# Kernel tuning notes

Hardware: AMD Instinct MI355X
Metric: run time of the kernel (lower is better)

## Reference

```python
import jax, jax.numpy as jnp
import numpy as np

N = 100_000   # nodes
E = 1_600_000 # edges
D = 32        # input_channels
H = 32        # hidden_inputs
C = 8         # output_channels
G = 64        # graphs in batch


def setup_inputs() -> dict:
    key = jax.random.key(0)
    ks = jax.random.split(key, 12)
    inp = {
        "x": jax.random.normal(ks[0], (N, D), dtype=jnp.float32),
        "edge_idx": jax.random.randint(ks[1], (2, E), 0, N, dtype=jnp.int64 if jax.config.jax_enable_x64 else jnp.int32),
        "edge_weight": jax.random.uniform(ks[2], (E,), dtype=jnp.float32),
        "batch": jnp.sort(jax.random.randint(ks[3], (N,), 0, G, dtype=jnp.int32)),
        # GCNConv weights (PyG: out = A_hat @ (x W) + b)
        "W1": jax.random.normal(ks[4], (D, H), dtype=jnp.float32) / np.sqrt(D),
        "b1": jnp.zeros((H,), dtype=jnp.float32),
        "W2": jax.random.normal(ks[5], (H, H), dtype=jnp.float32) / np.sqrt(H),
        "b2": jnp.zeros((H,), dtype=jnp.float32),
        "W3": jax.random.normal(ks[6], (H, H), dtype=jnp.float32) / np.sqrt(H),
        "b3": jnp.zeros((H,), dtype=jnp.float32),
        "Wout": jax.random.normal(ks[7], (H, C), dtype=jnp.float32) / np.sqrt(H),
        "bout": jnp.zeros((C,), dtype=jnp.float32),
    }
    return inp


def _gcn_norm(edge_idx, edge_weight, n_nodes):
    """Add self-loops (weight 1) and compute symmetric normalization,
    matching torch_geometric gcn_norm(add_self_loops=True)."""
    loop = jnp.arange(n_nodes, dtype=edge_idx.dtype)
    row = jnp.concatenate([edge_idx[0], loop])          # source j
    col = jnp.concatenate([edge_idx[1], loop])          # target i
    w = jnp.concatenate([edge_weight, jnp.ones((n_nodes,), edge_weight.dtype)])
    deg = jax.ops.segment_sum(w, col, num_segments=n_nodes)  # in-degree of targets
    dinv = jnp.where(deg > 0, jax.lax.rsqrt(deg), 0.0)
    norm = dinv[row] * w * dinv[col]
    return row, col, norm


def _gcn_conv(x, W, b, row, col, norm, n_nodes):
    h = x @ W                                   # [N, H] small GEMM
    msg = h[row] * norm[:, None]                # gather + scale  [E+N, H]
    agg = jax.ops.segment_sum(msg, col, num_segments=n_nodes)  # scatter-add
    return agg + b


def reference(x, edge_idx, edge_weight, batch, W1, b1, W2, b2, W3, b3, Wout, bout):
    n = x.shape[0]
    row, col, norm = _gcn_norm(edge_idx, edge_weight, n)
    h = jax.nn.relu(_gcn_conv(x, W1, b1, row, col, norm, n))
    h = jax.nn.relu(_gcn_conv(h, W2, b2, row, col, norm, n))
    h = jax.nn.relu(_gcn_conv(h, W3, b3, row, col, norm, n))
    # global mean pool over graphs
    sums = jax.ops.segment_sum(h, batch, num_segments=G)          # [G, H]
    cnts = jax.ops.segment_sum(jnp.ones((n,), h.dtype), batch, num_segments=G)
    pooled = sums / jnp.maximum(cnts, 1.0)[:, None]
    # dropout is identity in eval mode
    logits = pooled @ Wout + bout
    return jax.nn.log_softmax(logits, axis=1)
```

## Files before the change

### kernel.cpp

```cpp
#include <hip/hip_runtime.h>
#include <math.h>

#define NN 100000
#define NE 1600000
#define HD 32
#define NG 64
#define NC 8

#define P 256
#define PART 391
#define SCAP 7000
#define CH 8192
#define NBIN ((NE + CH - 1) / CH)
#define GEMM0_BLOCKS32 (NN / 32)
#define NORM_BLOCKS (NN * 8 / 256)

__device__ __forceinline__ float bf2f(unsigned short u) {
    return __uint_as_float(((unsigned int)u) << 16);
}
__device__ __forceinline__ unsigned short f2bf(float f) {
    unsigned int b = __float_as_uint(f);
    b = (b + 0x7FFFu + ((b >> 16) & 1u)) >> 16;
    return (unsigned short)b;
}

#if __has_builtin(__builtin_amdgcn_cvt_pk_f32_fp8) && __has_builtin(__builtin_amdgcn_cvt_pk_fp8_f32)
#define FP8_HW 1
#else
#define FP8_HW 0
#endif

__device__ __forceinline__ float e4m3f_sw(unsigned u) {
    unsigned code = u & 0x7fu;
    unsigned e = code >> 3;
    float v;
    if (e == 0) v = (float)code * 0.001953125f;
    else v = __uint_as_float(((e + 120u) << 23) | ((code & 7u) << 20));
    return (u & 0x80u) ? -v : v;
}
__device__ __forceinline__ unsigned f2e4m3_sw(float f) {
    unsigned s = (__float_as_uint(f) >> 31) << 7;
    float a = fminf(fabsf(f), 448.0f);
    unsigned code;
    if (a >= 0.015625f) {
        unsigned x = __float_as_uint(a);
        x += 0x0007FFFFu + ((x >> 20) & 1u);
        code = (((x >> 23) - 120u) << 3) | ((x >> 20) & 7u);
    } else {
        code = (unsigned)__float2int_rn(a * 512.0f);
    }
    return s | code;
}

__device__ __forceinline__ float4 fp8x4f(unsigned v) {
#if FP8_HW
    using floatx2 = __attribute__((ext_vector_type(2))) float;
    floatx2 lo = __builtin_amdgcn_cvt_pk_f32_fp8((int)v, false);
    floatx2 hi = __builtin_amdgcn_cvt_pk_f32_fp8((int)v, true);
    return make_float4(lo[0], lo[1], hi[0], hi[1]);
#else
    return make_float4(e4m3f_sw(v & 255), e4m3f_sw((v >> 8) & 255),
                       e4m3f_sw((v >> 16) & 255), e4m3f_sw(v >> 24));
#endif
}
__device__ __forceinline__ unsigned f4fp8(float a, float b, float c, float d) {
#if FP8_HW
    int pk = 0;
    pk = __builtin_amdgcn_cvt_pk_fp8_f32(a, b, pk, false);
    pk = __builtin_amdgcn_cvt_pk_fp8_f32(c, d, pk, true);
    return (unsigned)pk;
#else
    return f2e4m3_sw(a) | (f2e4m3_sw(b) << 8) | (f2e4m3_sw(c) << 16) | (f2e4m3_sw(d) << 24);
#endif
}

__global__ __launch_bounds__(1024) void k_bin_gemm0(const int* __restrict__ row,
                                                    const int* __restrict__ col,
                                                    const float* __restrict__ w,
                                                    int* __restrict__ pcnt,
                                                    uint2* __restrict__ staging,
                                                    const float* __restrict__ x,
                                                    const float* __restrict__ W1,
                                                    unsigned short* __restrict__ htmp) {
    int tid = threadIdx.x;
    if (blockIdx.x < NBIN) {
        __shared__ int hist[P];
        __shared__ int base_[P];
        int e0 = blockIdx.x * CH;
        int nrem = min(CH, NE - e0);
        if (tid < P) hist[tid] = 0;
        __syncthreads();
        for (int i = tid; i < nrem; i += 1024)
            atomicAdd(&hist[(unsigned)col[e0 + i] / PART], 1);
        __syncthreads();
        if (tid < P) {
            int h = hist[tid];
            base_[tid] = h ? atomicAdd(&pcnt[tid], h) : 0;
            hist[tid] = 0;
        }
        __syncthreads();
        for (int i = tid; i < nrem; i += 1024) {
            int c = col[e0 + i];
            int p = (unsigned)c / PART;
            int pos = base_[p] + atomicAdd(&hist[p], 1);
            uint2 v;
            v.x = (unsigned)(c - p * PART) | ((unsigned)row[e0 + i] << 9);
            v.y = __float_as_uint(w[e0 + i]);
            staging[(size_t)p * SCAP + pos] = v;
        }
    } else {
        __shared__ float sW[32 * 32];
        __shared__ float sX[32 * 32];
        int base = (blockIdx.x - NBIN) * 32;
        if (tid < 256) {
            ((float4*)sW)[tid] = ((const float4*)W1)[tid];
            ((float4*)sX)[tid] = ((const float4*)(x + (size_t)base * 32))[tid];
        }
        __syncthreads();
        int nl = tid >> 5, c = tid & 31;
        float acc = 0.0f;
#pragma unroll
        for (int k = 0; k < 32; ++k) acc = fmaf(sX[nl * 32 + k], sW[k * 32 + c], acc);
        htmp[(size_t)(base + nl) * 32 + c] = f2bf(acc);
    }
}

__global__ __launch_bounds__(512) void k_csr(const int* __restrict__ pcnt,
                                             const uint2* __restrict__ staging,
                                             int* __restrict__ off,
                                             int* __restrict__ cntg,
                                             float* __restrict__ dinv,
                                             const unsigned short* __restrict__ htmp,
                                             unsigned char* __restrict__ h1,
                                             unsigned* __restrict__ pairs) {
    __shared__ int spc[P];
    __shared__ int cnt_l[PART];
    __shared__ float wsum[PART];
    __shared__ int sc[PART];
    __shared__ float sdc[PART];
    __shared__ int cur[PART];
    int p = blockIdx.x, tid = threadIdx.x;
    if (tid < P) spc[tid] = pcnt[tid];
    __syncthreads();
#pragma unroll
    for (int d = 1; d < P; d <<= 1) {
        int t = 0;
        if (tid < P && tid >= d) t = spc[tid - d];
        __syncthreads();
        if (tid < P) spc[tid] += t;
        __syncthreads();
    }
    int m = pcnt[p];
    int pb = (p > 0) ? spc[p - 1] : 0;
    for (int i = tid; i < PART; i += 512) { cnt_l[i] = 0; wsum[i] = 0.0f; }
    __syncthreads();
    const uint2* st = staging + (size_t)p * SCAP;
    for (int i = tid; i < m; i += 512) {
        uint2 v = st[i];
        int cl = v.x & 511;
        atomicAdd(&cnt_l[cl], 1);
        atomicAdd(&wsum[cl], __uint_as_float(v.y));
    }
    __syncthreads();
    for (int i = tid; i < PART; i += 512) sc[i] = cnt_l[i];
    __syncthreads();
#pragma unroll
    for (int d = 1; d < 512; d <<= 1) {
        int t = 0;
        if (tid < PART && tid >= d) t = sc[tid - d];
        __syncthreads();
        if (tid < PART) sc[tid] += t;
        __syncthreads();
    }
    for (int i = tid; i < PART; i += 512) {
        int excl = sc[i] - cnt_l[i];
        cur[i] = excl;
        float dv = rsqrtf(1.0f + wsum[i]);
        sdc[i] = dv;
        int n = p * PART + i;
        if (n < NN) {
            off[n] = pb + excl;
            cntg[n] = cnt_l[i];
            dinv[n] = dv;
        }
    }
    __syncthreads();
    for (int u = tid; u < PART * 8; u += 512) {
        int i = u >> 3, q = u & 7;
        int n = p * PART + i;
        if (n < NN) {
            ushort4 hv = *((const ushort4*)(htmp + (size_t)n * 32) + q);
            float dv = sdc[i];
            *(unsigned*)(h1 + (size_t)n * 32 + q * 4) =
                f4fp8(dv * bf2f(hv.x), dv * bf2f(hv.y), dv * bf2f(hv.z), dv * bf2f(hv.w));
        }
    }
    unsigned* pr = pairs + pb;
    for (int ib = tid; ib < m; ib += 512 * 4) {
        uint2 v[4];
#pragma unroll
        for (int j = 0; j < 4; ++j) {
            int i = ib + j * 512;
            if (i < m) v[j] = st[i];
        }
#pragma unroll
        for (int j = 0; j < 4; ++j) {
            int i = ib + j * 512;
            if (i < m) {
                int cl = v[j].x & 511;
                int pos = atomicAdd(&cur[cl], 1);
                unsigned q = (unsigned)__float2int_rn(__uint_as_float(v[j].y) * 32768.0f);
                q = min(q, 32767u);
                pr[pos] = ((v[j].x >> 9) << 15) | q;
            }
        }
    }
}

#define NM_SCALE 3.0517578125e-5f
template <int MODE>
__global__ __launch_bounds__(256) void k_gather(const unsigned char* __restrict__ hb,
                                                const int* __restrict__ off,
                                                const int* __restrict__ cntg,
                                                const float* __restrict__ dinv,
                                                const unsigned* __restrict__ pairs,
                                                const float* __restrict__ bias,
                                                const float* __restrict__ Wn,
                                                unsigned char* __restrict__ hout,
                                                unsigned short* __restrict__ h3out) {
    __shared__ float sW[32 * 32];
    __shared__ float srow[32 * 33];
    int tid = threadIdx.x;
    if (MODE == 0) ((float4*)sW)[tid] = ((const float4*)Wn)[tid];
    int t = blockIdx.x * 256 + tid;
    int n = t >> 3, c4 = t & 7;
    int cn = cntg[n];
    const unsigned* pp = pairs + off[n];
    float di = dinv[n];
    unsigned hu = *(const unsigned*)(hb + (size_t)n * 32 + c4 * 4);
    float4 acc = fp8x4f(hu);
    int k = 0;
    for (; k + 8 <= cn; k += 8) {
        unsigned p[8];
#pragma unroll
        for (int j = 0; j < 8; ++j) p[j] = pp[k + j];
        unsigned v[8];
#pragma unroll
        for (int j = 0; j < 8; ++j)
            v[j] = *(const unsigned*)(hb + (size_t)(p[j] >> 15) * 32 + c4 * 4);
#pragma unroll
        for (int j = 0; j < 8; ++j) {
            float nm = (float)(p[j] & 32767u) * NM_SCALE;
            float4 f = fp8x4f(v[j]);
            acc.x = fmaf(nm, f.x, acc.x);
            acc.y = fmaf(nm, f.y, acc.y);
            acc.z = fmaf(nm, f.z, acc.z);
            acc.w = fmaf(nm, f.w, acc.w);
        }
    }
    for (; k + 4 <= cn; k += 4) {
        unsigned p[4];
#pragma unroll
        for (int j = 0; j < 4; ++j) p[j] = pp[k + j];
        unsigned v[4];
#pragma unroll
        for (int j = 0; j < 4; ++j)
            v[j] = *(const unsigned*)(hb + (size_t)(p[j] >> 15) * 32 + c4 * 4);
#pragma unroll
        for (int j = 0; j < 4; ++j) {
            float nm = (float)(p[j] & 32767u) * NM_SCALE;
            float4 f = fp8x4f(v[j]);
            acc.x = fmaf(nm, f.x, acc.x);
            acc.y = fmaf(nm, f.y, acc.y);
            acc.z = fmaf(nm, f.z, acc.z);
            acc.w = fmaf(nm, f.w, acc.w);
        }
    }
    for (; k < cn; ++k) {
        unsigned p = pp[k];
        unsigned v = *(const unsigned*)(hb + (size_t)(p >> 15) * 32 + c4 * 4);
        float nm = (float)(p & 32767u) * NM_SCALE;
        float4 f = fp8x4f(v);
        acc.x = fmaf(nm, f.x, acc.x);
        acc.y = fmaf(nm, f.y, acc.y);
        acc.z = fmaf(nm, f.z, acc.z);
        acc.w = fmaf(nm, f.w, acc.w);
    }
    int cb = c4 * 4;
    if (MODE == 0) {
        int ln = tid >> 3;
        srow[ln * 33 + cb + 0] = fmaxf(fmaf(di, acc.x, bias[cb + 0]), 0.0f);
        srow[ln * 33 + cb + 1] = fmaxf(fmaf(di, acc.y, bias[cb + 1]), 0.0f);
        srow[ln * 33 + cb + 2] = fmaxf(fmaf(di, acc.z, bias[cb + 2]), 0.0f);
        srow[ln * 33 + cb + 3] = fmaxf(fmaf(di, acc.w, bias[cb + 3]), 0.0f);
        __syncthreads();
        const float* rw = srow + ln * 33;
        float o0 = 0.f, o1 = 0.f, o2 = 0.f, o3 = 0.f;
#pragma unroll
        for (int kk = 0; kk < 32; ++kk) {
            float r = rw[kk];
            const float* wr = sW + kk * 32 + cb;
            o0 = fmaf(r, wr[0], o0);
            o1 = fmaf(r, wr[1], o1);
            o2 = fmaf(r, wr[2], o2);
            o3 = fmaf(r, wr[3], o3);
        }
        *(unsigned*)(hout + (size_t)n * 32 + cb) = f4fp8(di * o0, di * o1, di * o2, di * o3);
    } else {
        ushort4 ou;
        ou.x = f2bf(fmaxf(fmaf(di, acc.x, bias[cb + 0]), 0.0f));
        ou.y = f2bf(fmaxf(fmaf(di, acc.y, bias[cb + 1]), 0.0f));
        ou.z = f2bf(fmaxf(fmaf(di, acc.z, bias[cb + 2]), 0.0f));
        ou.w = f2bf(fmaxf(fmaf(di, acc.w, bias[cb + 3]), 0.0f));
        *((ushort4*)(h3out + (size_t)n * 32) + c4) = ou;
    }
}

__global__ __launch_bounds__(1024) void k_pool_head(const unsigned short* __restrict__ h3,
                                                    const int* __restrict__ batch,
                                                    const float* __restrict__ Wout,
                                                    const float* __restrict__ bout,
                                                    float* __restrict__ out) {
    int g = blockIdx.x;
    __shared__ int sb[2];
    if (threadIdx.x == 0) {
        int lo = 0, hi = NN;
        while (lo < hi) { int m = (lo + hi) >> 1; if (batch[m] < g) lo = m + 1; else hi = m; }
        sb[0] = lo;
        lo = 0; hi = NN;
        while (lo < hi) { int m = (lo + hi) >> 1; if (batch[m] < g + 1) lo = m + 1; else hi = m; }
        sb[1] = lo;
    }
    __syncthreads();
    int start = sb[0], end = sb[1];
    int c = threadIdx.x & 31, grp = threadIdx.x >> 5;
    float acc = 0.0f;
    for (int n = start + grp; n < end; n += 32)
        acc += bf2f(h3[(size_t)n * 32 + c]);
    __shared__ float red[32 * 32];
    red[grp * 32 + c] = acc;
    __syncthreads();
    __shared__ float pooled[32];
    if (threadIdx.x < 32) {
        float s = 0.0f;
#pragma unroll
        for (int gr = 0; gr < 32; ++gr) s += red[gr * 32 + threadIdx.x];
        pooled[threadIdx.x] = s / fmaxf((float)(end - start), 1.0f);
    }
    __syncthreads();
    __shared__ float slog[8];
    if (threadIdx.x < 8) {
        float l = bout[threadIdx.x];
#pragma unroll
        for (int k = 0; k < 32; ++k) l = fmaf(pooled[k], Wout[k * 8 + threadIdx.x], l);
        slog[threadIdx.x] = l;
    }
    __syncthreads();
    if (threadIdx.x < 8) {
        float m = slog[0];
#pragma unroll
        for (int i = 1; i < 8; ++i) m = fmaxf(m, slog[i]);
        float s = 0.0f;
#pragma unroll
        for (int i = 0; i < 8; ++i) s += expf(slog[i] - m);
        out[g * NC + threadIdx.x] = slog[threadIdx.x] - m - logf(s);
    }
}

extern "C" void kernel_launch(void* const* d_in, const int* in_sizes, int n_in,
                              void* d_out, int out_size, void* d_ws, size_t ws_size,
                              hipStream_t stream) {
    const float* x     = (const float*)d_in[0];
    const int*   eidx  = (const int*)d_in[1];
    const float* ew    = (const float*)d_in[2];
    const int*   batch = (const int*)d_in[3];
    const float* W1 = (const float*)d_in[4];
    const float* b1 = (const float*)d_in[5];
    const float* W2 = (const float*)d_in[6];
    const float* b2 = (const float*)d_in[7];
    const float* W3 = (const float*)d_in[8];
    const float* b3 = (const float*)d_in[9];
    const float* Wout = (const float*)d_in[10];
    const float* bout = (const float*)d_in[11];
    float* out = (float*)d_out;

    const int* row = eidx;
    const int* col = eidx + NE;

    unsigned char* h1 = (unsigned char*)d_ws;
    unsigned char* h2 = h1 + (size_t)NN * HD;
    unsigned short* h3 = (unsigned short*)(h2 + (size_t)NN * HD);
    unsigned* pairs = (unsigned*)(h3 + (size_t)NN * HD);
    uint2* staging = (uint2*)(pairs + NE);
    float* dinv = (float*)(staging + (size_t)P * SCAP);
    int* off  = (int*)(dinv + NN);
    int* cntg = off + NN;
    int* pcnt = cntg + NN;

    hipMemsetAsync(pcnt, 0, P * sizeof(int), stream);
    k_bin_gemm0<<<NBIN + GEMM0_BLOCKS32, 1024, 0, stream>>>(row, col, ew, pcnt, staging,
                                                            x, W1, h3 );
    k_csr<<<P, 512, 0, stream>>>(pcnt, staging, off, cntg, dinv, h3 , h1, pairs);
    k_gather<0><<<NORM_BLOCKS, 256, 0, stream>>>(h1, off, cntg, dinv, pairs, b1, W2,
                                                 h2, nullptr);
    k_gather<0><<<NORM_BLOCKS, 256, 0, stream>>>(h2, off, cntg, dinv, pairs, b2, W3,
                                                 h1, nullptr);
    k_gather<1><<<NORM_BLOCKS, 256, 0, stream>>>(h1, off, cntg, dinv, pairs, b3, nullptr,
                                                 nullptr, h3);
    k_pool_head<<<NG, 1024, 0, stream>>>(h3, batch, Wout, bout, out);
}
```

Baseline: 126.2 us.

## Stage gather pairs in LDS, cache bin columns, split pooling across blocks

Each gather block now loads its contiguous run of CSR pairs into shared memory in one coalesced pass, then reads neighbor indices from LDS, with a fallback to global when a block's edge count exceeds capacity. The binning kernel keeps the column indices in shared memory so they are not read from global a second time. Pooling is split into eight slices per graph that combine through atomics, followed by a separate single-block head kernel, which raises pooling parallelism at the cost of an extra launch and float atomics that make the summation order nondeterministic. The offset array gains a sentinel entry and the workspace layout shifts to make room for it.

```diff
diff --git a/kernel.cpp b/kernel.cpp
--- a/kernel.cpp
+++ b/kernel.cpp
@@ -14,6 +14,7 @@
 #define NBIN ((NE + CH - 1) / CH)
 #define GEMM0_BLOCKS32 (NN / 32)
 #define NORM_BLOCKS (NN * 8 / 256)
+#define CAPL 1024
 
 __device__ __forceinline__ float bf2f(unsigned short u) {
     return __uint_as_float(((unsigned int)u) << 16);
@@ -84,14 +85,18 @@
                                                     unsigned short* __restrict__ htmp) {
     int tid = threadIdx.x;
     if (blockIdx.x < NBIN) {
+        __shared__ int scol[CH];
         __shared__ int hist[P];
         __shared__ int base_[P];
         int e0 = blockIdx.x * CH;
         int nrem = min(CH, NE - e0);
         if (tid < P) hist[tid] = 0;
         __syncthreads();
-        for (int i = tid; i < nrem; i += 1024)
-            atomicAdd(&hist[(unsigned)col[e0 + i] / PART], 1);
+        for (int i = tid; i < nrem; i += 1024) {
+            int c = col[e0 + i];
+            scol[i] = c;
+            atomicAdd(&hist[(unsigned)c / PART], 1);
+        }
         __syncthreads();
         if (tid < P) {
             int h = hist[tid];
@@ -100,7 +105,7 @@
         }
         __syncthreads();
         for (int i = tid; i < nrem; i += 1024) {
-            int c = col[e0 + i];
+            int c = scol[i];
             int p = (unsigned)c / PART;
             int pos = base_[p] + atomicAdd(&hist[p], 1);
             uint2 v;
@@ -152,6 +157,7 @@
     }
     int m = pcnt[p];
     int pb = (p > 0) ? spc[p - 1] : 0;
+    if (p == P - 1 && tid == 0) off[NN] = pb + m;
     for (int i = tid; i < PART; i += 512) { cnt_l[i] = 0; wsum[i] = 0.0f; }
     __syncthreads();
     const uint2* st = staging + (size_t)p * SCAP;
@@ -218,6 +224,55 @@
 }
 
 #define NM_SCALE 3.0517578125e-5f
+
+#define GBODY(PAIR_AT)                                                              \
+    {                                                                               \
+        int k = 0;                                                                  \
+        for (; k + 8 <= cn; k += 8) {                                               \
+            unsigned pw[8];                                                         \
+            _Pragma("unroll") for (int j = 0; j < 8; ++j) pw[j] = PAIR_AT(k + j);   \
+            unsigned hv[8];                                                         \
+            _Pragma("unroll") for (int j = 0; j < 8; ++j)                           \
+                hv[j] = *(const unsigned*)(hb + (size_t)(pw[j] >> 15) * 32 + c4 * 4);\
+            _Pragma("unroll") for (int j = 0; j < 8; ++j) {                         \
+                float nm = (float)(pw[j] & 32767u) * NM_SCALE;                      \
+                float4 f = fp8x4f(hv[j]);                                           \
+                acc.x = fmaf(nm, f.x, acc.x);                                       \
+                acc.y = fmaf(nm, f.y, acc.y);                                       \
+                acc.z = fmaf(nm, f.z, acc.z);                                       \
+                acc.w = fmaf(nm, f.w, acc.w);                                       \
+            }                                                                       \
+        }                                                                           \
+        for (; k + 4 <= cn; k += 4) {                                               \
+            unsigned pw[4];                                                         \
+            _Pragma("unroll") for (int j = 0; j < 4; ++j) pw[j] = PAIR_AT(k + j);   \
+            unsigned hv[4];                                                         \
+            _Pragma("unroll") for (int j = 0; j < 4; ++j)                           \
+                hv[j] = *(const unsigned*)(hb + (size_t)(pw[j] >> 15) * 32 + c4 * 4);\
+            _Pragma("unroll") for (int j = 0; j < 4; ++j) {                         \
+                float nm = (float)(pw[j] & 32767u) * NM_SCALE;                      \
+                float4 f = fp8x4f(hv[j]);                                           \
+                acc.x = fmaf(nm, f.x, acc.x);                                       \
+                acc.y = fmaf(nm, f.y, acc.y);                                       \
+                acc.z = fmaf(nm, f.z, acc.z);                                       \
+                acc.w = fmaf(nm, f.w, acc.w);                                       \
+            }                                                                       \
+        }                                                                           \
+        for (; k < cn; ++k) {                                                       \
+            unsigned pw = PAIR_AT(k);                                               \
+            unsigned hv = *(const unsigned*)(hb + (size_t)(pw >> 15) * 32 + c4 * 4);\
+            float nm = (float)(pw & 32767u) * NM_SCALE;                             \
+            float4 f = fp8x4f(hv);                                                  \
+            acc.x = fmaf(nm, f.x, acc.x);                                           \
+            acc.y = fmaf(nm, f.y, acc.y);                                           \
+            acc.z = fmaf(nm, f.z, acc.z);                                           \
+            acc.w = fmaf(nm, f.w, acc.w);                                           \
+        }                                                                           \
+    }
+
+#define SPAIR_AT(i) spair[l0 + (i)]
+#define GPAIR_AT(i) pp[(i)]
+
 template <int MODE>
 __global__ __launch_bounds__(256) void k_gather(const unsigned char* __restrict__ hb,
                                                 const int* __restrict__ off,
@@ -230,61 +285,28 @@
                                                 unsigned short* __restrict__ h3out) {
     __shared__ float sW[32 * 32];
     __shared__ float srow[32 * 33];
+    __shared__ unsigned spair[CAPL];
     int tid = threadIdx.x;
     if (MODE == 0) ((float4*)sW)[tid] = ((const float4*)Wn)[tid];
+    int nb = blockIdx.x * 32;
+    int base = off[nb];
+    int mb = off[nb + 32] - base;
+    int mbc = min(mb, CAPL);
+    for (int i = tid; i < mbc; i += 256) spair[i] = pairs[base + i];
+    __syncthreads();
     int t = blockIdx.x * 256 + tid;
     int n = t >> 3, c4 = t & 7;
     int cn = cntg[n];
-    const unsigned* pp = pairs + off[n];
+    int offn = off[n];
+    int l0 = offn - base;
+    const unsigned* pp = pairs + offn;
     float di = dinv[n];
     unsigned hu = *(const unsigned*)(hb + (size_t)n * 32 + c4 * 4);
     float4 acc = fp8x4f(hu);
-    int k = 0;
-    for (; k + 8 <= cn; k += 8) {
-        unsigned p[8];
-#pragma unroll
-        for (int j = 0; j < 8; ++j) p[j] = pp[k + j];
-        unsigned v[8];
-#pragma unroll
-        for (int j = 0; j < 8; ++j)
-            v[j] = *(const unsigned*)(hb + (size_t)(p[j] >> 15) * 32 + c4 * 4);
-#pragma unroll
-        for (int j = 0; j < 8; ++j) {
-            float nm = (float)(p[j] & 32767u) * NM_SCALE;
-            float4 f = fp8x4f(v[j]);
-            acc.x = fmaf(nm, f.x, acc.x);
-            acc.y = fmaf(nm, f.y, acc.y);
-            acc.z = fmaf(nm, f.z, acc.z);
-            acc.w = fmaf(nm, f.w, acc.w);
-        }
-    }
-    for (; k + 4 <= cn; k += 4) {
-        unsigned p[4];
-#pragma unroll
-        for (int j = 0; j < 4; ++j) p[j] = pp[k + j];
-        unsigned v[4];
-#pragma unroll
-        for (int j = 0; j < 4; ++j)
-            v[j] = *(const unsigned*)(hb + (size_t)(p[j] >> 15) * 32 + c4 * 4);
-#pragma unroll
-        for (int j = 0; j < 4; ++j) {
-            float nm = (float)(p[j] & 32767u) * NM_SCALE;
-            float4 f = fp8x4f(v[j]);
-            acc.x = fmaf(nm, f.x, acc.x);
-            acc.y = fmaf(nm, f.y, acc.y);
-            acc.z = fmaf(nm, f.z, acc.z);
-            acc.w = fmaf(nm, f.w, acc.w);
-        }
-    }
-    for (; k < cn; ++k) {
-        unsigned p = pp[k];
-        unsigned v = *(const unsigned*)(hb + (size_t)(p >> 15) * 32 + c4 * 4);
-        float nm = (float)(p & 32767u) * NM_SCALE;
-        float4 f = fp8x4f(v);
-        acc.x = fmaf(nm, f.x, acc.x);
-        acc.y = fmaf(nm, f.y, acc.y);
-        acc.z = fmaf(nm, f.z, acc.z);
-        acc.w = fmaf(nm, f.w, acc.w);
+    if (l0 + cn <= CAPL) {
+        GBODY(SPAIR_AT)
+    } else {
+        GBODY(GPAIR_AT)
     }
     int cb = c4 * 4;
     if (MODE == 0) {
@@ -316,12 +338,11 @@
     }
 }
 
-__global__ __launch_bounds__(1024) void k_pool_head(const unsigned short* __restrict__ h3,
-                                                    const int* __restrict__ batch,
-                                                    const float* __restrict__ Wout,
-                                                    const float* __restrict__ bout,
-                                                    float* __restrict__ out) {
-    int g = blockIdx.x;
+__global__ __launch_bounds__(1024) void k_pool(const unsigned short* __restrict__ h3,
+                                               const int* __restrict__ batch,
+                                               float* __restrict__ gsum,
+                                               float* __restrict__ gcnt) {
+    int g = blockIdx.x >> 3, s = blockIdx.x & 7;
     __shared__ int sb[2];
     if (threadIdx.x == 0) {
         int lo = 0, hi = NN;
@@ -332,38 +353,60 @@
         sb[1] = lo;
     }
     __syncthreads();
-    int start = sb[0], end = sb[1];
+    int start = sb[0], len = sb[1] - sb[0];
+    int a = start + (int)((long long)len * s / 8);
+    int b = start + (int)((long long)len * (s + 1) / 8);
     int c = threadIdx.x & 31, grp = threadIdx.x >> 5;
     float acc = 0.0f;
-    for (int n = start + grp; n < end; n += 32)
+    for (int n = a + grp; n < b; n += 32)
         acc += bf2f(h3[(size_t)n * 32 + c]);
     __shared__ float red[32 * 32];
     red[grp * 32 + c] = acc;
     __syncthreads();
-    __shared__ float pooled[32];
     if (threadIdx.x < 32) {
+        float sum = 0.0f;
+#pragma unroll
+        for (int gr = 0; gr < 32; ++gr) sum += red[gr * 32 + threadIdx.x];
+        if (sum != 0.0f) atomicAdd(&gsum[g * HD + threadIdx.x], sum);
+    }
+    if (threadIdx.x == 0 && b > a) atomicAdd(&gcnt[g], (float)(b - a));
+}
+
+__global__ __launch_bounds__(256) void k_head(const float* __restrict__ gsum,
+                                              const float* __restrict__ gcnt,
+                                              const float* __restrict__ Wout,
+                                              const float* __restrict__ bout,
+                                              float* __restrict__ out) {
+    __shared__ float pooled[NG * 33];
+    __shared__ float sW[32 * NC];
+    __shared__ float slog[NG * NC];
+    int tid = threadIdx.x;
+    sW[tid] = Wout[tid];
+    for (int i = tid; i < NG * HD; i += 256) {
+        int g = i >> 5, c = i & 31;
+        pooled[g * 33 + c] = gsum[i] / fmaxf(gcnt[g], 1.0f);
+    }
+    __syncthreads();
+    for (int i = tid; i < NG * NC; i += 256) {
+        int g = i >> 3, c = i & 7;
+        float l = bout[c];
+        const float* pr = pooled + g * 33;
+#pragma unroll
+        for (int k = 0; k < 32; ++k) l = fmaf(pr[k], sW[k * NC + c], l);
+        slog[i] = l;
+    }
+    __syncthreads();
+    if (tid < NG) {
+        const float* sl = slog + tid * NC;
+        float m = sl[0];
+#pragma unroll
+        for (int i = 1; i < NC; ++i) m = fmaxf(m, sl[i]);
         float s = 0.0f;
 #pragma unroll
-        for (int gr = 0; gr < 32; ++gr) s += red[gr * 32 + threadIdx.x];
-        pooled[threadIdx.x] = s / fmaxf((float)(end - start), 1.0f);
-    }
-    __syncthreads();
-    __shared__ float slog[8];
-    if (threadIdx.x < 8) {
-        float l = bout[threadIdx.x];
-#pragma unroll
-        for (int k = 0; k < 32; ++k) l = fmaf(pooled[k], Wout[k * 8 + threadIdx.x], l);
-        slog[threadIdx.x] = l;
-    }
-    __syncthreads();
-    if (threadIdx.x < 8) {
-        float m = slog[0];
-#pragma unroll
-        for (int i = 1; i < 8; ++i) m = fmaxf(m, slog[i]);
-        float s = 0.0f;
-#pragma unroll
-        for (int i = 0; i < 8; ++i) s += expf(slog[i] - m);
-        out[g * NC + threadIdx.x] = slog[threadIdx.x] - m - logf(s);
+        for (int i = 0; i < NC; ++i) s += expf(sl[i] - m);
+        float lse = m + logf(s);
+#pragma unroll
+        for (int i = 0; i < NC; ++i) out[tid * NC + i] = sl[i] - lse;
     }
 }
 
@@ -394,10 +437,12 @@
     uint2* staging = (uint2*)(pairs + NE);
     float* dinv = (float*)(staging + (size_t)P * SCAP);
     int* off  = (int*)(dinv + NN);
-    int* cntg = off + NN;
+    int* cntg = off + NN + 1;
     int* pcnt = cntg + NN;
-
-    hipMemsetAsync(pcnt, 0, P * sizeof(int), stream);
+    float* gsum = (float*)(pcnt + P);
+    float* gcnt = gsum + NG * HD;
+
+    hipMemsetAsync(pcnt, 0, (P + NG * HD + NG) * sizeof(int), stream);
     k_bin_gemm0<<<NBIN + GEMM0_BLOCKS32, 1024, 0, stream>>>(row, col, ew, pcnt, staging,
                                                             x, W1, h3 );
     k_csr<<<P, 512, 0, stream>>>(pcnt, staging, off, cntg, dinv, h3 , h1, pairs);
@@ -407,5 +452,6 @@
                                                  h1, nullptr);
     k_gather<1><<<NORM_BLOCKS, 256, 0, stream>>>(h1, off, cntg, dinv, pairs, b3, nullptr,
                                                  nullptr, h3);
-    k_pool_head<<<NG, 1024, 0, stream>>>(h3, batch, Wout, bout, out);
-}
+    k_pool<<<NG * 8, 1024, 0, stream>>>(h3, batch, gsum, gcnt);
+    k_head<<<1, 256, 0, stream>>>(gsum, gcnt, Wout, bout, out);
+}
```

Result: faster. 123.2 us (-2.4%).
